# Performance work log

Measured on AMD Instinct MI355X. Metric: run time of the kernel, lower is better.

## Reference

```python
import jax, jax.numpy as jnp
import numpy as np

N, E, CLIP, HID, H, P, MD, B = 4096, 16384, 512, 1024, 4, 4, 512, 32
OUT2 = P * MD  # 2048


def prelu(x, a):
    return jnp.where(x >= 0, x, a * x)


def add_self_loops(src, dst, edge_attr, n):
    # PyG fill_value='mean': self-loop edge_attr = mean of incoming edge attrs
    sums = jax.ops.segment_sum(edge_attr, dst, num_segments=n)
    cnt = jax.ops.segment_sum(jnp.ones((dst.shape[0], 1), edge_attr.dtype), dst, num_segments=n)
    loop_attr = sums / jnp.maximum(cnt, 1.0)
    idx = jnp.arange(n)
    return (jnp.concatenate([src, idx]), jnp.concatenate([dst, idx]),
            jnp.concatenate([edge_attr, loop_attr], axis=0))


def gat_conv(x, src, dst, edge_attr, W, asrc, adst, We, ae, bias, heads, c):
    # PyG GATConv, concat=False (mean over heads), edge_dim used only in attention
    n = x.shape[0]
    src, dst, edge_attr = add_self_loops(src, dst, edge_attr, n)
    h = (x @ W).reshape(n, heads, c)                      # [N,H,C]
    e = (edge_attr @ We).reshape(-1, heads, c)            # [E',H,C]
    a_s = jnp.einsum('nhc,hc->nh', h, asrc)
    a_d = jnp.einsum('nhc,hc->nh', h, adst)
    a_e = jnp.einsum('ehc,hc->eh', e, ae)
    alpha = jax.nn.leaky_relu(a_s[src] + a_d[dst] + a_e, 0.2)  # [E',H]
    amax = jax.ops.segment_max(alpha, dst, num_segments=n)
    ex = jnp.exp(alpha - amax[dst])
    denom = jax.ops.segment_sum(ex, dst, num_segments=n)
    w = ex / jnp.maximum(denom[dst], 1e-16)
    msg = h[src] * w[:, :, None]                          # [E',H,C]
    out = jax.ops.segment_sum(msg, dst, num_segments=n)   # [N,H,C]
    return out.mean(axis=1) + bias


def attentional_pool(x, batch, gW1, gb1, gp1, gW2, gb2, gp2, gW3, gb3, n_graphs):
    gate = prelu(x @ gW1 + gb1, gp1)
    gate = prelu(gate @ gW2 + gb2, gp2)
    gate = gate @ gW3 + gb3                               # [N,1]
    gmax = jax.ops.segment_max(gate, batch, num_segments=n_graphs)
    ex = jnp.exp(gate - gmax[batch])
    denom = jax.ops.segment_sum(ex, batch, num_segments=n_graphs)
    s = ex / jnp.maximum(denom[batch], 1e-16)             # [N,1]
    return jax.ops.segment_sum(s * x, batch, num_segments=n_graphs)  # [B,F]


def setup_inputs() -> dict:
    key = jax.random.key(0)
    ks = jax.random.split(key, 24)
    sc = 0.05
    inp = {
        'x': jax.random.normal(ks[0], (N, CLIP), jnp.float32),
        'edge_index': jax.random.randint(ks[1], (2, E), 0, N),
        'edge_attr': jax.random.normal(ks[2], (E, CLIP), jnp.float32),
        'batch': jnp.sort(jax.random.randint(ks[3], (N,), 0, B)),
        # GATConv 1
        'W1': jax.random.normal(ks[4], (CLIP, H * HID), jnp.float32) * sc,
        'asrc1': jax.random.normal(ks[5], (H, HID), jnp.float32) * sc,
        'adst1': jax.random.normal(ks[6], (H, HID), jnp.float32) * sc,
        'We1': jax.random.normal(ks[7], (CLIP, H * HID), jnp.float32) * sc,
        'ae1': jax.random.normal(ks[8], (H, HID), jnp.float32) * sc,
        'b1': jnp.zeros((HID,), jnp.float32),
        'p1': jnp.float32(0.25),
        # GATConv 2
        'W2': jax.random.normal(ks[9], (HID, H * OUT2), jnp.float32) * sc,
        'asrc2': jax.random.normal(ks[10], (H, OUT2), jnp.float32) * sc,
        'adst2': jax.random.normal(ks[11], (H, OUT2), jnp.float32) * sc,
        'We2': jax.random.normal(ks[12], (CLIP, H * OUT2), jnp.float32) * sc,
        'ae2': jax.random.normal(ks[13], (H, OUT2), jnp.float32) * sc,
        'b2': jnp.zeros((OUT2,), jnp.float32),
        'p2': jnp.float32(0.25),
        # AttentionalAggregation gate_nn
        'gW1': jax.random.normal(ks[14], (OUT2, HID), jnp.float32) * sc,
        'gb1': jnp.zeros((HID,), jnp.float32),
        'gp1': jnp.float32(0.25),
        'gW2': jax.random.normal(ks[15], (HID, HID), jnp.float32) * sc,
        'gb2': jnp.zeros((HID,), jnp.float32),
        'gp2': jnp.float32(0.25),
        'gW3': jax.random.normal(ks[16], (HID, 1), jnp.float32) * sc,
        'gb3': jnp.zeros((1,), jnp.float32),
    }
    return inp


def reference(x, edge_index, edge_attr, batch,
              W1, asrc1, adst1, We1, ae1, b1, p1,
              W2, asrc2, adst2, We2, ae2, b2, p2,
              gW1, gb1, gp1, gW2, gb2, gp2, gW3, gb3):
    src, dst = edge_index[0], edge_index[1]
    h = gat_conv(x, src, dst, edge_attr, W1, asrc1, adst1, We1, ae1, b1, H, HID)
    h = prelu(h, p1)
    h = gat_conv(h, src, dst, edge_attr, W2, asrc2, adst2, We2, ae2, b2, H, OUT2)
    h = prelu(h, p2)
    pooled = attentional_pool(h, batch, gW1, gb1, gp1, gW2, gb2, gp2, gW3, gb3, B)
    return pooled.reshape(-1, P, MD)  # [B, prefix_length, mbart_dim]
```

## Files before the change

### kernel.cpp

```cpp
#include <hip/hip_runtime.h>
#include <hip/hip_bf16.h>
#include <math.h>

#define N_NODES 4096
#define N_EDGES 16384
#define CLIPD   512
#define HID     1024
#define NH      4
#define OUTD    2048
#define NB      32

typedef __bf16 bf16_t;
typedef bf16_t bf16x8 __attribute__((ext_vector_type(8)));
typedef float f32x4 __attribute__((ext_vector_type(4)));

static __device__ __forceinline__ float lrelu(float x) { return x >= 0.f ? x : 0.2f * x; }

static __device__ __forceinline__ unsigned short f2bf(float f) {
  union { float f; unsigned int u; } v; v.f = f;
  unsigned int u = v.u;
  unsigned int r = (u + 0x7FFFu + ((u >> 16) & 1u)) >> 16;
  return (unsigned short)r;
}
static __device__ __forceinline__ float bf2f(unsigned short u) {
  union { unsigned int i; float f; } v; v.i = ((unsigned int)u) << 16; return v.f;
}

#define GLDS(g, l) __builtin_amdgcn_global_load_lds( \
    (const __attribute__((address_space(1))) void*)(g), \
    (__attribute__((address_space(3))) void*)(l), 16, 0, 0)

__device__ __forceinline__ void stcvt_tile(float (*t)[33], const float* __restrict__ in,
                                           unsigned short* __restrict__ out,
                                           int K1, int N1, int NHH, int h, int bx, int by,
                                           float scale) {
  const int k0 = by * 32, n0 = bx * 32;
  const int tx = threadIdx.x, ty = threadIdx.y;
#pragma unroll
  for (int i = 0; i < 4; ++i)
    t[ty + 8 * i][tx] = in[(size_t)(k0 + ty + 8 * i) * (NHH * N1) + (size_t)h * N1 + n0 + tx];
  __syncthreads();
#pragma unroll
  for (int i = 0; i < 4; ++i)
    out[(size_t)(n0 + ty + 8 * i) * (NHH * K1) + (size_t)h * K1 + k0 + tx] =
        f2bf(scale * t[tx][ty + 8 * i]);
}

__global__ __launch_bounds__(256) void wprep_kernel(const float* __restrict__ W1, const float* __restrict__ W2,
                                                    const float* __restrict__ gW1, const float* __restrict__ gW2,
                                                    unsigned short* __restrict__ B1t, unsigned short* __restrict__ B2t,
                                                    unsigned short* __restrict__ gW1t, unsigned short* __restrict__ gW2t) {
  __shared__ float t[32][33];
  const int id = blockIdx.x;
  if (id < 2048) {
    int h = id >> 9, r = id & 511;
    stcvt_tile(t, W1, B1t, CLIPD, HID, NH, h, r & 31, r >> 5, 0.25f);
  } else if (id < 10240) {
    int r2 = id - 2048;
    int h = r2 >> 11, r = r2 & 2047;
    stcvt_tile(t, W2, B2t, HID, OUTD, NH, h, r & 63, r >> 6, 0.25f);
  } else if (id < 12288) {
    int r = id - 10240;
    stcvt_tile(t, gW1, gW1t, OUTD, HID, 1, 0, r & 31, r >> 5, 1.0f);
  } else {
    int r = id - 12288;
    stcvt_tile(t, gW2, gW2t, HID, HID, 1, 0, r & 31, r >> 5, 1.0f);
  }
}

__device__ __forceinline__ void vfold(float (*r1)[NH], float (*r2)[NH],
                                      const float* __restrict__ W,
                                      const float* __restrict__ a1v, const float* __restrict__ a2v,
                                      float* __restrict__ o1, float* __restrict__ o2, int C, int k) {
  const int tid = threadIdx.x;
  const float* row = W + (size_t)k * (NH * C);
  float x1[NH] = {0.f, 0.f, 0.f, 0.f}, x2[NH] = {0.f, 0.f, 0.f, 0.f};
  for (int c = tid; c < C; c += 256) {
    for (int h = 0; h < NH; ++h) {
      float w = row[h * C + c];
      x1[h] += w * a1v[h * C + c];
      x2[h] += w * a2v[h * C + c];
    }
  }
  for (int h = 0; h < NH; ++h)
    for (int o = 32; o > 0; o >>= 1) {
      x1[h] += __shfl_down(x1[h], o);
      x2[h] += __shfl_down(x2[h], o);
    }
  const int wid = tid >> 6, lane = tid & 63;
  if (lane == 0)
    for (int h = 0; h < NH; ++h) { r1[wid][h] = x1[h]; r2[wid][h] = x2[h]; }
  __syncthreads();
  if (tid < NH)
    o1[k * NH + tid] = r1[0][tid] + r1[1][tid] + r1[2][tid] + r1[3][tid];
  else if (o2 != nullptr && tid < 2 * NH) {
    int h = tid - NH;
    o2[k * NH + h] = r2[0][h] + r2[1][h] + r2[2][h] + r2[3][h];
  }
}

__global__ __launch_bounds__(256) void vprep_kernel(const float* __restrict__ We1, const float* __restrict__ ae1w,
                                                    const float* __restrict__ We2, const float* __restrict__ ae2w,
                                                    const float* __restrict__ W1, const float* __restrict__ asrc1,
                                                    const float* __restrict__ adst1,
                                                    const float* __restrict__ W2, const float* __restrict__ asrc2,
                                                    const float* __restrict__ adst2,
                                                    float* __restrict__ v1, float* __restrict__ v2,
                                                    float* __restrict__ us1, float* __restrict__ ud1,
                                                    float* __restrict__ us2, float* __restrict__ ud2) {
  __shared__ float r1[4][NH], r2[4][NH];
  const int id = blockIdx.x;
  if (id < 512)       vfold(r1, r2, We1, ae1w, ae1w, v1, nullptr, HID, id);
  else if (id < 1024) vfold(r1, r2, We2, ae2w, ae2w, v2, nullptr, OUTD, id - 512);
  else if (id < 1536) vfold(r1, r2, W1, asrc1, adst1, us1, ud1, HID, id - 1024);
  else                vfold(r1, r2, W2, asrc2, adst2, us2, ud2, OUTD, id - 1536);
}

__global__ __launch_bounds__(1024) void csr_kernel(const int* __restrict__ ei,
                                                   int* __restrict__ offs,
                                                   int* __restrict__ csr_src, int* __restrict__ csr_eid) {
  __shared__ int sdeg[N_NODES];
  __shared__ int soffs[N_NODES];
  __shared__ int sscan[1024];
  const int t = threadIdx.x;
  for (int i = t; i < N_NODES; i += 1024) sdeg[i] = 0;
  __syncthreads();
  for (int e = t; e < N_EDGES; e += 1024) atomicAdd(&sdeg[ei[N_EDGES + e]], 1);
  __syncthreads();
  const int d0 = sdeg[4 * t], d1 = sdeg[4 * t + 1], d2 = sdeg[4 * t + 2], d3 = sdeg[4 * t + 3];
  sscan[t] = d0 + d1 + d2 + d3;
  __syncthreads();
  for (int off = 1; off < 1024; off <<= 1) {
    int v = (t >= off) ? sscan[t - off] : 0;
    __syncthreads();
    sscan[t] += v;
    __syncthreads();
  }
  const int base = (t > 0) ? sscan[t - 1] : 0;
  soffs[4 * t] = base;
  soffs[4 * t + 1] = base + d0;
  soffs[4 * t + 2] = base + d0 + d1;
  soffs[4 * t + 3] = base + d0 + d1 + d2;
#pragma unroll
  for (int j = 0; j < 4; ++j) offs[4 * t + j] = soffs[4 * t + j];
  if (t == 1023) offs[N_NODES] = sscan[1023];
  sdeg[4 * t] = 0; sdeg[4 * t + 1] = 0; sdeg[4 * t + 2] = 0; sdeg[4 * t + 3] = 0;
  __syncthreads();
  for (int e = t; e < N_EDGES; e += 1024) {
    int dst = ei[N_EDGES + e];
    int pos = soffs[dst] + atomicAdd(&sdeg[dst], 1);
    csr_src[pos] = ei[e];
    csr_eid[pos] = e;
  }
}

__global__ __launch_bounds__(256) void ae_kernel(const float* __restrict__ ea, const int* __restrict__ ei,
                                                 const float* __restrict__ v1, const float* __restrict__ v2,
                                                 float* __restrict__ ae1, float* __restrict__ ae2,
                                                 float* __restrict__ aesum1, float* __restrict__ aesum2) {
  __shared__ float4 v1s[CLIPD];
  __shared__ float4 v2s[CLIPD];
  const int tid = threadIdx.x;
  v1s[tid] = ((const float4*)v1)[tid];
  v1s[tid + 256] = ((const float4*)v1)[tid + 256];
  v2s[tid] = ((const float4*)v2)[tid];
  v2s[tid + 256] = ((const float4*)v2)[tid + 256];
  __syncthreads();
  const int wid = tid >> 6, lane = tid & 63;
  for (int i = 0; i < 16; ++i) {
    const int e = blockIdx.x * 64 + wid * 16 + i;
    const float* row = ea + (size_t)e * CLIPD;
    float a1[NH] = {0.f, 0.f, 0.f, 0.f}, a2[NH] = {0.f, 0.f, 0.f, 0.f};
    for (int k = lane; k < CLIPD; k += 64) {
      float x = row[k];
      float4 w1 = v1s[k];
      float4 w2 = v2s[k];
      a1[0] += x * w1.x; a1[1] += x * w1.y; a1[2] += x * w1.z; a1[3] += x * w1.w;
      a2[0] += x * w2.x; a2[1] += x * w2.y; a2[2] += x * w2.z; a2[3] += x * w2.w;
    }
    for (int h = 0; h < NH; ++h)
      for (int o = 32; o > 0; o >>= 1) {
        a1[h] += __shfl_down(a1[h], o);
        a2[h] += __shfl_down(a2[h], o);
      }
    if (lane == 0) {
      int dst = ei[N_EDGES + e];
      for (int h = 0; h < NH; ++h) {
        ae1[e * NH + h] = a1[h];
        ae2[e * NH + h] = a2[h];
        atomicAdd(&aesum1[dst * NH + h], a1[h]);
        atomicAdd(&aesum2[dst * NH + h], a2[h]);
      }
    }
  }
}

__global__ __launch_bounds__(256) void xprep_kernel(const float* __restrict__ x,
                                                    const float* __restrict__ us, const float* __restrict__ ud,
                                                    unsigned short* __restrict__ xb,
                                                    float* __restrict__ as_, float* __restrict__ ad_) {
  __shared__ float4 su[CLIPD], sd[CLIPD];
  const int tid = threadIdx.x;
  for (int k = tid; k < CLIPD; k += 256) {
    su[k] = ((const float4*)us)[k];
    sd[k] = ((const float4*)ud)[k];
  }
  __syncthreads();
  const int wid = tid >> 6, lane = tid & 63;
  const int n = blockIdx.x * 4 + wid;
  const float* row = x + (size_t)n * CLIPD;
  unsigned short* orow = xb + (size_t)n * CLIPD;
  float s[NH] = {0.f, 0.f, 0.f, 0.f}, d[NH] = {0.f, 0.f, 0.f, 0.f};
  for (int q = lane; q < CLIPD / 4; q += 64) {
    float4 xv = ((const float4*)row)[q];
    ushort4 ob;
    ob.x = f2bf(xv.x); ob.y = f2bf(xv.y); ob.z = f2bf(xv.z); ob.w = f2bf(xv.w);
    ((ushort4*)orow)[q] = ob;
    const float* xp = &xv.x;
#pragma unroll
    for (int j = 0; j < 4; ++j) {
      float xs = xp[j];
      float4 u = su[q * 4 + j], v = sd[q * 4 + j];
      s[0] += xs * u.x; s[1] += xs * u.y; s[2] += xs * u.z; s[3] += xs * u.w;
      d[0] += xs * v.x; d[1] += xs * v.y; d[2] += xs * v.z; d[3] += xs * v.w;
    }
  }
#pragma unroll
  for (int h = 0; h < NH; ++h)
    for (int o = 32; o > 0; o >>= 1) {
      s[h] += __shfl_down(s[h], o);
      d[h] += __shfl_down(d[h], o);
    }
  if (lane == 0)
    for (int h = 0; h < NH; ++h) {
      as_[n * NH + h] = s[h];
      ad_[n * NH + h] = d[h];
    }
}

__global__ __launch_bounds__(256) void rowdot_o(const unsigned short* __restrict__ rows,
                                                const float* __restrict__ us, const float* __restrict__ ud,
                                                float* __restrict__ as_, float* __restrict__ ad_) {
  __shared__ float4 su[HID], sd[HID];
  const int tid = threadIdx.x;
  for (int k = tid; k < HID; k += 256) {
    su[k] = ((const float4*)us)[k];
    sd[k] = ((const float4*)ud)[k];
  }
  __syncthreads();
  const int wid = tid >> 6, lane = tid & 63;
  const int n = blockIdx.x * 4 + wid;
  const unsigned short* row = rows + (size_t)n * HID;
  float s[NH] = {0.f, 0.f, 0.f, 0.f}, d[NH] = {0.f, 0.f, 0.f, 0.f};
  for (int k2 = lane; k2 < HID / 2; k2 += 64) {
    ushort2 uv = ((const ushort2*)row)[k2];
    float f0 = bf2f(uv.x), f1 = bf2f(uv.y);
    float4 u0 = su[2 * k2], u1 = su[2 * k2 + 1];
    float4 v0 = sd[2 * k2], v1 = sd[2 * k2 + 1];
    s[0] += f0 * u0.x + f1 * u1.x; s[1] += f0 * u0.y + f1 * u1.y;
    s[2] += f0 * u0.z + f1 * u1.z; s[3] += f0 * u0.w + f1 * u1.w;
    d[0] += f0 * v0.x + f1 * v1.x; d[1] += f0 * v0.y + f1 * v1.y;
    d[2] += f0 * v0.z + f1 * v1.z; d[3] += f0 * v0.w + f1 * v1.w;
  }
#pragma unroll
  for (int h = 0; h < NH; ++h)
    for (int o = 32; o > 0; o >>= 1) {
      s[h] += __shfl_down(s[h], o);
      d[h] += __shfl_down(d[h], o);
    }
  if (lane == 0)
    for (int h = 0; h < NH; ++h) {
      as_[n * NH + h] = s[h];
      ad_[n * NH + h] = d[h];
    }
}

template<int C>
__global__ __launch_bounds__(256) void aggn_kernel(const unsigned short* __restrict__ src,
                                                   const float* __restrict__ as_, const float* __restrict__ ad_,
                                                   const float* __restrict__ aee, const float* __restrict__ aesum,
                                                   const int* __restrict__ offs, const int* __restrict__ csr_src,
                                                   const int* __restrict__ csr_eid,
                                                   unsigned short* __restrict__ out) {
  constexpr int CPT = C / 256;
  const int n = blockIdx.x;
  const int tid = threadIdx.x;
  const int off = offs[n];
  const int deg = offs[n + 1] - off;
  __shared__ float minv[NH], dinv[NH], wself[NH];
  __shared__ float wch[32][NH];
  __shared__ int sch[32];
  if (tid < 64) {
    const int h = tid >> 4, slot = tid & 15;
    const float adn = ad_[n * NH + h];
    const float aself = lrelu(as_[n * NH + h] + adn + aesum[n * NH + h] / fmaxf((float)deg, 1.f));
    float m = (slot == 0) ? aself : -3.0e38f;
    for (int i = slot; i < deg; i += 16) {
      float a = lrelu(as_[csr_src[off + i] * NH + h] + adn + aee[csr_eid[off + i] * NH + h]);
      m = fmaxf(m, a);
    }
    for (int o = 1; o < 16; o <<= 1) m = fmaxf(m, __shfl_xor(m, o));
    float den = (slot == 0) ? __expf(aself - m) : 0.f;
    for (int i = slot; i < deg; i += 16) {
      float a = lrelu(as_[csr_src[off + i] * NH + h] + adn + aee[csr_eid[off + i] * NH + h]);
      den += __expf(a - m);
    }
    for (int o = 1; o < 16; o <<= 1) den += __shfl_xor(den, o);
    if (slot == 0) {
      minv[h] = m;
      dinv[h] = 1.0f / den;
      wself[h] = __expf(aself - m) / den;
    }
  }
  __syncthreads();
  float acc[NH][CPT];
#pragma unroll
  for (int h = 0; h < NH; ++h)
#pragma unroll
    for (int c = 0; c < CPT; ++c) acc[h][c] = 0.f;
  for (int base = 0; base < deg; base += 32) {
    const int cnt = min(32, deg - base);
    if (tid < cnt * NH) {
      const int i = tid >> 2, h = tid & 3;
      const int sidx = csr_src[off + base + i];
      float a = lrelu(as_[sidx * NH + h] + ad_[n * NH + h] + aee[csr_eid[off + base + i] * NH + h]);
      wch[i][h] = __expf(a - minv[h]) * dinv[h];
      if (h == 0) sch[i] = sidx;
    }
    __syncthreads();
    for (int i = 0; i < cnt; ++i) {
      const unsigned short* hp = src + (size_t)sch[i] * C + tid * CPT;
      float f[CPT];
      if constexpr (CPT == 2) {
        ushort2 u = *(const ushort2*)hp;
        f[0] = bf2f(u.x); f[1] = bf2f(u.y);
      } else {
        ushort4 u = *(const ushort4*)hp;
        f[0] = bf2f(u.x); f[1] = bf2f(u.y); f[2] = bf2f(u.z); f[3] = bf2f(u.w);
      }
#pragma unroll
      for (int h = 0; h < NH; ++h) {
        const float wv = wch[i][h];
#pragma unroll
        for (int c = 0; c < CPT; ++c) acc[h][c] += wv * f[c];
      }
    }
    __syncthreads();
  }
  {
    const unsigned short* hp = src + (size_t)n * C + tid * CPT;
    float f[CPT];
    if constexpr (CPT == 2) {
      ushort2 u = *(const ushort2*)hp;
      f[0] = bf2f(u.x); f[1] = bf2f(u.y);
    } else {
      ushort4 u = *(const ushort4*)hp;
      f[0] = bf2f(u.x); f[1] = bf2f(u.y); f[2] = bf2f(u.z); f[3] = bf2f(u.w);
    }
#pragma unroll
    for (int h = 0; h < NH; ++h) {
      const float wv = wself[h];
#pragma unroll
      for (int c = 0; c < CPT; ++c) acc[h][c] += wv * f[c];
    }
  }
#pragma unroll
  for (int h = 0; h < NH; ++h) {
    if constexpr (CPT == 2) {
      ushort2 o;
      o.x = f2bf(acc[h][0]); o.y = f2bf(acc[h][1]);
      *(ushort2*)&out[((size_t)n * NH + h) * C + tid * 2] = o;
    } else {
      ushort4 o;
      o.x = f2bf(acc[h][0]); o.y = f2bf(acc[h][1]); o.z = f2bf(acc[h][2]); o.w = f2bf(acc[h][3]);
      *(ushort4*)&out[((size_t)n * NH + h) * C + tid * 4] = o;
    }
  }
}

template<int EPI, int WF, int BN>
__global__ __launch_bounds__(256) void mfma_gemm(const unsigned short* __restrict__ A,
                                                 const unsigned short* __restrict__ Bt,
                                                 unsigned short* __restrict__ C,
                                                 float* __restrict__ Cf,
                                                 int M, int N, int K,
                                                 const float* __restrict__ bias,
                                                 const float* __restrict__ pa) {
  constexpr int NFR = BN / 32;
  __shared__ unsigned short As[128 * 32];
  __shared__ unsigned short Bs[BN * 32];
  const int nwg = gridDim.x * gridDim.y;
  int id = blockIdx.y * gridDim.x + blockIdx.x;
  id = (id & 7) * (nwg >> 3) + (id >> 3);
  const int bx = id % gridDim.x, by = id / gridDim.x;
  const int tid = threadIdx.x;
  const int lane = tid & 63;
  const int w = tid >> 6;
  const int wr = w >> 1, wc = w & 1;
  const int brow = by * 128, bcol = bx * BN;
  const int r0 = tid >> 2;
  const int koff = (tid & 3) * 8;
  const int fr = lane & 15;
  const int fk = (lane >> 4) * 8;
  f32x4 acc[4][NFR] = {};
  for (int kt = 0; kt < K; kt += 32) {
    GLDS(A + (size_t)(brow + r0) * K + kt + koff, &As[tid * 8]);
    GLDS(A + (size_t)(brow + 64 + r0) * K + kt + koff, &As[2048 + tid * 8]);
    GLDS(Bt + (size_t)(bcol + r0) * K + kt + koff, &Bs[tid * 8]);
    if constexpr (BN == 128)
      GLDS(Bt + (size_t)(bcol + 64 + r0) * K + kt + koff, &Bs[2048 + tid * 8]);
    asm volatile("s_waitcnt vmcnt(0)" ::: "memory");
    __syncthreads();
    bf16x8 af[4], bfr[NFR];
#pragma unroll
    for (int mi = 0; mi < 4; ++mi)
      af[mi] = *(const bf16x8*)&As[(wr * 64 + mi * 16 + fr) * 32 + fk];
#pragma unroll
    for (int ni = 0; ni < NFR; ++ni)
      bfr[ni] = *(const bf16x8*)&Bs[(wc * (BN / 2) + ni * 16 + fr) * 32 + fk];
#pragma unroll
    for (int mi = 0; mi < 4; ++mi)
#pragma unroll
      for (int ni = 0; ni < NFR; ++ni)
        acc[mi][ni] = __builtin_amdgcn_mfma_f32_16x16x32_bf16(af[mi], bfr[ni], acc[mi][ni], 0, 0, 0);
    __syncthreads();
  }
  const float ap = EPI ? *pa : 0.f;
#pragma unroll
  for (int mi = 0; mi < 4; ++mi) {
    const int rb = brow + wr * 64 + mi * 16 + (lane >> 4) * 4;
#pragma unroll
    for (int ni = 0; ni < NFR; ++ni) {
      const int col = bcol + wc * (BN / 2) + ni * 16 + fr;
      float bv = 0.f;
      if (EPI) bv = bias[col];
#pragma unroll
      for (int r = 0; r < 4; ++r) {
        float v = acc[mi][ni][r];
        if (EPI) { v += bv; v = v >= 0.f ? v : ap * v; }
        C[(size_t)(rb + r) * N + col] = f2bf(v);
        if (WF) Cf[(size_t)(rb + r) * N + col] = v;
      }
    }
  }
}

__global__ __launch_bounds__(256) void gate3_kernel(const unsigned short* __restrict__ gh2,
                                                    const float* __restrict__ gW3,
                                                    const float* __restrict__ gb3, float* __restrict__ gate) {
  const int n = blockIdx.x, tid = threadIdx.x;
  const unsigned short* row = gh2 + (size_t)n * HID;
  ushort4 u = *(const ushort4*)&row[tid * 4];
  float4 wv = *(const float4*)&gW3[tid * 4];
  float acc = bf2f(u.x) * wv.x + bf2f(u.y) * wv.y + bf2f(u.z) * wv.z + bf2f(u.w) * wv.w;
  for (int o = 32; o > 0; o >>= 1) acc += __shfl_down(acc, o);
  __shared__ float red[4];
  const int wid = tid >> 6, lane = tid & 63;
  if (lane == 0) red[wid] = acc;
  __syncthreads();
  if (tid == 0) gate[n] = red[0] + red[1] + red[2] + red[3] + gb3[0];
}

__global__ __launch_bounds__(256) void pool2_kernel(const float* __restrict__ out2,
                                                    const float* __restrict__ gate,
                                                    const int* __restrict__ batch,
                                                    float* __restrict__ dout) {
  const int b = blockIdx.y;
  const int tid = threadIdx.x;
  const int col = blockIdx.x * 256 + tid;
  int lo = 0, hi = N_NODES;
  while (lo < hi) { int mid = (lo + hi) >> 1; if (batch[mid] < b) lo = mid + 1; else hi = mid; }
  const int s = lo;
  hi = N_NODES;
  while (lo < hi) { int mid = (lo + hi) >> 1; if (batch[mid] < b + 1) lo = mid + 1; else hi = mid; }
  const int e = lo;
  __shared__ float red[4];
  const int wid = tid >> 6, lane = tid & 63;
  float m = -3.0e38f;
  for (int n = s + tid; n < e; n += 256) m = fmaxf(m, gate[n]);
  for (int o = 32; o > 0; o >>= 1) m = fmaxf(m, __shfl_down(m, o));
  if (lane == 0) red[wid] = m;
  __syncthreads();
  m = fmaxf(fmaxf(red[0], red[1]), fmaxf(red[2], red[3]));
  __syncthreads();
  float sum = 0.f;
  for (int n = s + tid; n < e; n += 256) sum += __expf(gate[n] - m);
  for (int o = 32; o > 0; o >>= 1) sum += __shfl_down(sum, o);
  if (lane == 0) red[wid] = sum;
  __syncthreads();
  sum = red[0] + red[1] + red[2] + red[3];
  const float gi = 1.0f / fmaxf(sum, 1e-16f);
  float acc = 0.f;
  for (int n = s; n < e; ++n)
    acc += __expf(gate[n] - m) * gi * out2[(size_t)n * OUTD + col];
  dout[(size_t)b * OUTD + col] = acc;
}

#define MB(x) ((size_t)(x) * 1048576)
#define WS_XB     MB(0)
#define WS_B1T    MB(4)
#define WS_B2T    MB(8)
#define WS_GW1T   MB(24)
#define WS_GW2T   MB(28)
#define WS_AGGX   MB(30)
#define WS_OUT1B  MB(46)
#define WS_AGGO   MB(54)
#define WS_OUT2F  MB(86)
#define WS_OUT2B  MB(118)
#define WS_GH1B   MB(134)
#define WS_GH2B   MB(142)
#define WS_SM     MB(150)
#define WS_AES1   (WS_SM + 0)
#define WS_AES2   (WS_AES1 + 65536)
#define WS_OFFS   (WS_AES2 + 65536)
#define WS_CSRS   (WS_OFFS + 16640)
#define WS_CSRE   (WS_CSRS + 65536)
#define WS_AS1    (WS_CSRE + 65536)
#define WS_AD1    (WS_AS1 + 65536)
#define WS_AEE1   (WS_AD1 + 65536)
#define WS_AS2    (WS_AEE1 + 262144)
#define WS_AD2    (WS_AS2 + 65536)
#define WS_AEE2   (WS_AD2 + 65536)
#define WS_V1     (WS_AEE2 + 262144)
#define WS_V2     (WS_V1 + 8192)
#define WS_US1    (WS_V2 + 8192)
#define WS_UD1    (WS_US1 + 8192)
#define WS_US2    (WS_UD1 + 8192)
#define WS_UD2    (WS_US2 + 16384)
#define WS_GATE   (WS_UD2 + 16384)

extern "C" void kernel_launch(void* const* d_in, const int* in_sizes, int n_in,
                              void* d_out, int out_size, void* d_ws, size_t ws_size,
                              hipStream_t stream) {
  const float* x     = (const float*)d_in[0];
  const int*   ei    = (const int*)d_in[1];
  const float* ea    = (const float*)d_in[2];
  const int*   batch = (const int*)d_in[3];
  const float* W1    = (const float*)d_in[4];
  const float* asrc1 = (const float*)d_in[5];
  const float* adst1 = (const float*)d_in[6];
  const float* We1   = (const float*)d_in[7];
  const float* ae1w  = (const float*)d_in[8];
  const float* b1    = (const float*)d_in[9];
  const float* p1    = (const float*)d_in[10];
  const float* W2    = (const float*)d_in[11];
  const float* asrc2 = (const float*)d_in[12];
  const float* adst2 = (const float*)d_in[13];
  const float* We2   = (const float*)d_in[14];
  const float* ae2w  = (const float*)d_in[15];
  const float* b2    = (const float*)d_in[16];
  const float* p2    = (const float*)d_in[17];
  const float* gW1   = (const float*)d_in[18];
  const float* gb1   = (const float*)d_in[19];
  const float* gp1   = (const float*)d_in[20];
  const float* gW2   = (const float*)d_in[21];
  const float* gb2   = (const float*)d_in[22];
  const float* gp2   = (const float*)d_in[23];
  const float* gW3   = (const float*)d_in[24];
  const float* gb3   = (const float*)d_in[25];

  char* ws = (char*)d_ws;
  unsigned short* xb    = (unsigned short*)(ws + WS_XB);
  unsigned short* B1t   = (unsigned short*)(ws + WS_B1T);
  unsigned short* B2t   = (unsigned short*)(ws + WS_B2T);
  unsigned short* gW1t  = (unsigned short*)(ws + WS_GW1T);
  unsigned short* gW2t  = (unsigned short*)(ws + WS_GW2T);
  unsigned short* aggXb = (unsigned short*)(ws + WS_AGGX);
  unsigned short* out1b = (unsigned short*)(ws + WS_OUT1B);
  unsigned short* aggOb = (unsigned short*)(ws + WS_AGGO);
  float*          out2f = (float*)(ws + WS_OUT2F);
  unsigned short* out2b = (unsigned short*)(ws + WS_OUT2B);
  unsigned short* gh1b  = (unsigned short*)(ws + WS_GH1B);
  unsigned short* gh2b  = (unsigned short*)(ws + WS_GH2B);
  float* aesum1  = (float*)(ws + WS_AES1);
  float* aesum2  = (float*)(ws + WS_AES2);
  int*   offs    = (int*)(ws + WS_OFFS);
  int*   csr_src = (int*)(ws + WS_CSRS);
  int*   csr_eid = (int*)(ws + WS_CSRE);
  float* as1     = (float*)(ws + WS_AS1);
  float* ad1     = (float*)(ws + WS_AD1);
  float* aee1    = (float*)(ws + WS_AEE1);
  float* as2     = (float*)(ws + WS_AS2);
  float* ad2     = (float*)(ws + WS_AD2);
  float* aee2    = (float*)(ws + WS_AEE2);
  float* v1      = (float*)(ws + WS_V1);
  float* v2      = (float*)(ws + WS_V2);
  float* us1     = (float*)(ws + WS_US1);
  float* ud1     = (float*)(ws + WS_UD1);
  float* us2     = (float*)(ws + WS_US2);
  float* ud2     = (float*)(ws + WS_UD2);
  float* gate    = (float*)(ws + WS_GATE);
  float* dout    = (float*)d_out;

  hipMemsetAsync(ws + WS_AES1, 0, 131072, stream);

  wprep_kernel<<<13312, dim3(32, 8), 0, stream>>>(W1, W2, gW1, gW2, B1t, B2t, gW1t, gW2t);
  vprep_kernel<<<2560, 256, 0, stream>>>(We1, ae1w, We2, ae2w, W1, asrc1, adst1, W2, asrc2, adst2,
                                         v1, v2, us1, ud1, us2, ud2);
  csr_kernel<<<1, 1024, 0, stream>>>(ei, offs, csr_src, csr_eid);
  ae_kernel<<<N_EDGES / 64, 256, 0, stream>>>(ea, ei, v1, v2, aee1, aee2, aesum1, aesum2);
  xprep_kernel<<<N_NODES / 4, 256, 0, stream>>>(x, us1, ud1, xb, as1, ad1);

  aggn_kernel<CLIPD><<<N_NODES, 256, 0, stream>>>(xb, as1, ad1, aee1, aesum1, offs, csr_src, csr_eid, aggXb);
  mfma_gemm<1, 0, 64><<<dim3(HID / 64, N_NODES / 128), 256, 0, stream>>>(
      aggXb, B1t, out1b, nullptr, N_NODES, HID, NH * CLIPD, b1, p1);

  rowdot_o<<<N_NODES / 4, 256, 0, stream>>>(out1b, us2, ud2, as2, ad2);
  aggn_kernel<HID><<<N_NODES, 256, 0, stream>>>(out1b, as2, ad2, aee2, aesum2, offs, csr_src, csr_eid, aggOb);
  mfma_gemm<1, 1, 128><<<dim3(OUTD / 128, N_NODES / 128), 256, 0, stream>>>(
      aggOb, B2t, out2b, out2f, N_NODES, OUTD, NH * HID, b2, p2);

  mfma_gemm<1, 0, 64><<<dim3(HID / 64, N_NODES / 128), 256, 0, stream>>>(
      out2b, gW1t, gh1b, nullptr, N_NODES, HID, OUTD, gb1, gp1);
  mfma_gemm<1, 0, 64><<<dim3(HID / 64, N_NODES / 128), 256, 0, stream>>>(
      gh1b, gW2t, gh2b, nullptr, N_NODES, HID, HID, gb2, gp2);
  gate3_kernel<<<N_NODES, 256, 0, stream>>>(gh2b, gW3, gb3, gate);

  pool2_kernel<<<dim3(OUTD / 256, NB), 256, 0, stream>>>(out2f, gate, batch, dout);
}
```

Before: 543.7 us.

## Merge prep kernels, wave-per-node aggregation, fuse gate projection into GEMM epilogue

Merges the weight-transpose and vector-fold prep kernels into one launch, and the edge-attention and x-prep kernels into another. Node aggregation now uses one wave per node with 16-byte bf16 loads instead of a 256-thread block with LDS staging and barriers. The final 1-wide gate projection is folded into the second gate GEMM's epilogue through shuffle reductions and atomicAdd, which removes the gh2 buffer and the gate3 kernel. The gb3 bias is dropped because the pooling softmax does not change under a constant shift. The second GAT GEMM tile width also changes from 128 to 64. These changes target launch count, extra memory traffic and per-node sync cost, at the price of float atomic contention on the gate values and possibly lower GEMM reuse.

```diff
diff --git a/kernel.cpp b/kernel.cpp
--- a/kernel.cpp
+++ b/kernel.cpp
@@ -13,6 +13,7 @@
 typedef __bf16 bf16_t;
 typedef bf16_t bf16x8 __attribute__((ext_vector_type(8)));
 typedef float f32x4 __attribute__((ext_vector_type(4)));
+typedef unsigned short u16x8 __attribute__((ext_vector_type(8)));
 
 static __device__ __forceinline__ float lrelu(float x) { return x >= 0.f ? x : 0.2f * x; }
 
@@ -35,7 +36,7 @@
                                            int K1, int N1, int NHH, int h, int bx, int by,
                                            float scale) {
   const int k0 = by * 32, n0 = bx * 32;
-  const int tx = threadIdx.x, ty = threadIdx.y;
+  const int tx = threadIdx.x & 31, ty = threadIdx.x >> 5;
 #pragma unroll
   for (int i = 0; i < 4; ++i)
     t[ty + 8 * i][tx] = in[(size_t)(k0 + ty + 8 * i) * (NHH * N1) + (size_t)h * N1 + n0 + tx];
@@ -44,28 +45,6 @@
   for (int i = 0; i < 4; ++i)
     out[(size_t)(n0 + ty + 8 * i) * (NHH * K1) + (size_t)h * K1 + k0 + tx] =
         f2bf(scale * t[tx][ty + 8 * i]);
-}
-
-__global__ __launch_bounds__(256) void wprep_kernel(const float* __restrict__ W1, const float* __restrict__ W2,
-                                                    const float* __restrict__ gW1, const float* __restrict__ gW2,
-                                                    unsigned short* __restrict__ B1t, unsigned short* __restrict__ B2t,
-                                                    unsigned short* __restrict__ gW1t, unsigned short* __restrict__ gW2t) {
-  __shared__ float t[32][33];
-  const int id = blockIdx.x;
-  if (id < 2048) {
-    int h = id >> 9, r = id & 511;
-    stcvt_tile(t, W1, B1t, CLIPD, HID, NH, h, r & 31, r >> 5, 0.25f);
-  } else if (id < 10240) {
-    int r2 = id - 2048;
-    int h = r2 >> 11, r = r2 & 2047;
-    stcvt_tile(t, W2, B2t, HID, OUTD, NH, h, r & 63, r >> 6, 0.25f);
-  } else if (id < 12288) {
-    int r = id - 10240;
-    stcvt_tile(t, gW1, gW1t, OUTD, HID, 1, 0, r & 31, r >> 5, 1.0f);
-  } else {
-    int r = id - 12288;
-    stcvt_tile(t, gW2, gW2t, HID, HID, 1, 0, r & 31, r >> 5, 1.0f);
-  }
 }
 
 __device__ __forceinline__ void vfold(float (*r1)[NH], float (*r2)[NH],
@@ -99,21 +78,41 @@
   }
 }
 
-__global__ __launch_bounds__(256) void vprep_kernel(const float* __restrict__ We1, const float* __restrict__ ae1w,
-                                                    const float* __restrict__ We2, const float* __restrict__ ae2w,
-                                                    const float* __restrict__ W1, const float* __restrict__ asrc1,
-                                                    const float* __restrict__ adst1,
-                                                    const float* __restrict__ W2, const float* __restrict__ asrc2,
-                                                    const float* __restrict__ adst2,
-                                                    float* __restrict__ v1, float* __restrict__ v2,
-                                                    float* __restrict__ us1, float* __restrict__ ud1,
-                                                    float* __restrict__ us2, float* __restrict__ ud2) {
+__global__ __launch_bounds__(256) void prep_kernel(
+    const float* __restrict__ W1, const float* __restrict__ W2,
+    const float* __restrict__ gW1, const float* __restrict__ gW2,
+    unsigned short* __restrict__ B1t, unsigned short* __restrict__ B2t,
+    unsigned short* __restrict__ gW1t, unsigned short* __restrict__ gW2t,
+    const float* __restrict__ We1, const float* __restrict__ ae1w,
+    const float* __restrict__ We2, const float* __restrict__ ae2w,
+    const float* __restrict__ asrc1, const float* __restrict__ adst1,
+    const float* __restrict__ asrc2, const float* __restrict__ adst2,
+    float* __restrict__ v1, float* __restrict__ v2,
+    float* __restrict__ us1, float* __restrict__ ud1,
+    float* __restrict__ us2, float* __restrict__ ud2) {
+  __shared__ float t[32][33];
   __shared__ float r1[4][NH], r2[4][NH];
   const int id = blockIdx.x;
-  if (id < 512)       vfold(r1, r2, We1, ae1w, ae1w, v1, nullptr, HID, id);
-  else if (id < 1024) vfold(r1, r2, We2, ae2w, ae2w, v2, nullptr, OUTD, id - 512);
-  else if (id < 1536) vfold(r1, r2, W1, asrc1, adst1, us1, ud1, HID, id - 1024);
-  else                vfold(r1, r2, W2, asrc2, adst2, us2, ud2, OUTD, id - 1536);
+  if (id < 2048) {
+    int h = id >> 9, r = id & 511;
+    stcvt_tile(t, W1, B1t, CLIPD, HID, NH, h, r & 31, r >> 5, 0.25f);
+  } else if (id < 10240) {
+    int r2_ = id - 2048;
+    int h = r2_ >> 11, r = r2_ & 2047;
+    stcvt_tile(t, W2, B2t, HID, OUTD, NH, h, r & 63, r >> 6, 0.25f);
+  } else if (id < 12288) {
+    int r = id - 10240;
+    stcvt_tile(t, gW1, gW1t, OUTD, HID, 1, 0, r & 31, r >> 5, 1.0f);
+  } else if (id < 13312) {
+    int r = id - 12288;
+    stcvt_tile(t, gW2, gW2t, HID, HID, 1, 0, r & 31, r >> 5, 1.0f);
+  } else {
+    int vid = id - 13312;
+    if (vid < 512)       vfold(r1, r2, We1, ae1w, ae1w, v1, nullptr, HID, vid);
+    else if (vid < 1024) vfold(r1, r2, We2, ae2w, ae2w, v2, nullptr, OUTD, vid - 512);
+    else if (vid < 1536) vfold(r1, r2, W1, asrc1, adst1, us1, ud1, HID, vid - 1024);
+    else                 vfold(r1, r2, W2, asrc2, adst2, us2, ud2, OUTD, vid - 1536);
+  }
 }
 
 __global__ __launch_bounds__(1024) void csr_kernel(const int* __restrict__ ei,
@@ -154,88 +153,85 @@
   }
 }
 
-__global__ __launch_bounds__(256) void ae_kernel(const float* __restrict__ ea, const int* __restrict__ ei,
-                                                 const float* __restrict__ v1, const float* __restrict__ v2,
-                                                 float* __restrict__ ae1, float* __restrict__ ae2,
-                                                 float* __restrict__ aesum1, float* __restrict__ aesum2) {
-  __shared__ float4 v1s[CLIPD];
-  __shared__ float4 v2s[CLIPD];
+__global__ __launch_bounds__(256) void aexprep_kernel(
+    const float* __restrict__ ea, const int* __restrict__ ei,
+    const float* __restrict__ v1, const float* __restrict__ v2,
+    float* __restrict__ ae1, float* __restrict__ ae2,
+    float* __restrict__ aesum1, float* __restrict__ aesum2,
+    const float* __restrict__ x, const float* __restrict__ us, const float* __restrict__ ud,
+    unsigned short* __restrict__ xb, float* __restrict__ as_, float* __restrict__ ad_) {
+  __shared__ float4 s0[CLIPD];
+  __shared__ float4 s1[CLIPD];
   const int tid = threadIdx.x;
-  v1s[tid] = ((const float4*)v1)[tid];
-  v1s[tid + 256] = ((const float4*)v1)[tid + 256];
-  v2s[tid] = ((const float4*)v2)[tid];
-  v2s[tid + 256] = ((const float4*)v2)[tid + 256];
-  __syncthreads();
   const int wid = tid >> 6, lane = tid & 63;
-  for (int i = 0; i < 16; ++i) {
-    const int e = blockIdx.x * 64 + wid * 16 + i;
-    const float* row = ea + (size_t)e * CLIPD;
-    float a1[NH] = {0.f, 0.f, 0.f, 0.f}, a2[NH] = {0.f, 0.f, 0.f, 0.f};
-    for (int k = lane; k < CLIPD; k += 64) {
-      float x = row[k];
-      float4 w1 = v1s[k];
-      float4 w2 = v2s[k];
-      a1[0] += x * w1.x; a1[1] += x * w1.y; a1[2] += x * w1.z; a1[3] += x * w1.w;
-      a2[0] += x * w2.x; a2[1] += x * w2.y; a2[2] += x * w2.z; a2[3] += x * w2.w;
-    }
+  if (blockIdx.x < 256) {
+    s0[tid] = ((const float4*)v1)[tid];
+    s0[tid + 256] = ((const float4*)v1)[tid + 256];
+    s1[tid] = ((const float4*)v2)[tid];
+    s1[tid + 256] = ((const float4*)v2)[tid + 256];
+    __syncthreads();
+    for (int i = 0; i < 16; ++i) {
+      const int e = blockIdx.x * 64 + wid * 16 + i;
+      const float* row = ea + (size_t)e * CLIPD;
+      float a1[NH] = {0.f, 0.f, 0.f, 0.f}, a2[NH] = {0.f, 0.f, 0.f, 0.f};
+      for (int k = lane; k < CLIPD; k += 64) {
+        float xv = row[k];
+        float4 w1 = s0[k];
+        float4 w2 = s1[k];
+        a1[0] += xv * w1.x; a1[1] += xv * w1.y; a1[2] += xv * w1.z; a1[3] += xv * w1.w;
+        a2[0] += xv * w2.x; a2[1] += xv * w2.y; a2[2] += xv * w2.z; a2[3] += xv * w2.w;
+      }
+      for (int h = 0; h < NH; ++h)
+        for (int o = 32; o > 0; o >>= 1) {
+          a1[h] += __shfl_down(a1[h], o);
+          a2[h] += __shfl_down(a2[h], o);
+        }
+      if (lane == 0) {
+        int dst = ei[N_EDGES + e];
+        for (int h = 0; h < NH; ++h) {
+          ae1[e * NH + h] = a1[h];
+          ae2[e * NH + h] = a2[h];
+          atomicAdd(&aesum1[dst * NH + h], a1[h]);
+          atomicAdd(&aesum2[dst * NH + h], a2[h]);
+        }
+      }
+    }
+  } else {
+    for (int k = tid; k < CLIPD; k += 256) {
+      s0[k] = ((const float4*)us)[k];
+      s1[k] = ((const float4*)ud)[k];
+    }
+    __syncthreads();
+    const int n = (blockIdx.x - 256) * 4 + wid;
+    const float* row = x + (size_t)n * CLIPD;
+    unsigned short* orow = xb + (size_t)n * CLIPD;
+    float s[NH] = {0.f, 0.f, 0.f, 0.f}, d[NH] = {0.f, 0.f, 0.f, 0.f};
+    for (int q = lane; q < CLIPD / 4; q += 64) {
+      float4 xv = ((const float4*)row)[q];
+      ushort4 ob;
+      ob.x = f2bf(xv.x); ob.y = f2bf(xv.y); ob.z = f2bf(xv.z); ob.w = f2bf(xv.w);
+      ((ushort4*)orow)[q] = ob;
+      const float* xp = &xv.x;
+#pragma unroll
+      for (int j = 0; j < 4; ++j) {
+        float xs = xp[j];
+        float4 u = s0[q * 4 + j], v = s1[q * 4 + j];
+        s[0] += xs * u.x; s[1] += xs * u.y; s[2] += xs * u.z; s[3] += xs * u.w;
+        d[0] += xs * v.x; d[1] += xs * v.y; d[2] += xs * v.z; d[3] += xs * v.w;
+      }
+    }
+#pragma unroll
     for (int h = 0; h < NH; ++h)
       for (int o = 32; o > 0; o >>= 1) {
-        a1[h] += __shfl_down(a1[h], o);
-        a2[h] += __shfl_down(a2[h], o);
-      }
-    if (lane == 0) {
-      int dst = ei[N_EDGES + e];
+        s[h] += __shfl_down(s[h], o);
+        d[h] += __shfl_down(d[h], o);
+      }
+    if (lane == 0)
       for (int h = 0; h < NH; ++h) {
-        ae1[e * NH + h] = a1[h];
-        ae2[e * NH + h] = a2[h];
-        atomicAdd(&aesum1[dst * NH + h], a1[h]);
-        atomicAdd(&aesum2[dst * NH + h], a2[h]);
-      }
-    }
-  }
-}
-
-__global__ __launch_bounds__(256) void xprep_kernel(const float* __restrict__ x,
-                                                    const float* __restrict__ us, const float* __restrict__ ud,
-                                                    unsigned short* __restrict__ xb,
-                                                    float* __restrict__ as_, float* __restrict__ ad_) {
-  __shared__ float4 su[CLIPD], sd[CLIPD];
-  const int tid = threadIdx.x;
-  for (int k = tid; k < CLIPD; k += 256) {
-    su[k] = ((const float4*)us)[k];
-    sd[k] = ((const float4*)ud)[k];
-  }
-  __syncthreads();
-  const int wid = tid >> 6, lane = tid & 63;
-  const int n = blockIdx.x * 4 + wid;
-  const float* row = x + (size_t)n * CLIPD;
-  unsigned short* orow = xb + (size_t)n * CLIPD;
-  float s[NH] = {0.f, 0.f, 0.f, 0.f}, d[NH] = {0.f, 0.f, 0.f, 0.f};
-  for (int q = lane; q < CLIPD / 4; q += 64) {
-    float4 xv = ((const float4*)row)[q];
-    ushort4 ob;
-    ob.x = f2bf(xv.x); ob.y = f2bf(xv.y); ob.z = f2bf(xv.z); ob.w = f2bf(xv.w);
-    ((ushort4*)orow)[q] = ob;
-    const float* xp = &xv.x;
-#pragma unroll
-    for (int j = 0; j < 4; ++j) {
-      float xs = xp[j];
-      float4 u = su[q * 4 + j], v = sd[q * 4 + j];
-      s[0] += xs * u.x; s[1] += xs * u.y; s[2] += xs * u.z; s[3] += xs * u.w;
-      d[0] += xs * v.x; d[1] += xs * v.y; d[2] += xs * v.z; d[3] += xs * v.w;
-    }
-  }
-#pragma unroll
-  for (int h = 0; h < NH; ++h)
-    for (int o = 32; o > 0; o >>= 1) {
-      s[h] += __shfl_down(s[h], o);
-      d[h] += __shfl_down(d[h], o);
-    }
-  if (lane == 0)
-    for (int h = 0; h < NH; ++h) {
-      as_[n * NH + h] = s[h];
-      ad_[n * NH + h] = d[h];
-    }
+        as_[n * NH + h] = s[h];
+        ad_[n * NH + h] = d[h];
+      }
+  }
 }
 
 __global__ __launch_bounds__(256) void rowdot_o(const unsigned short* __restrict__ rows,
@@ -276,116 +272,107 @@
 }
 
 template<int C>
-__global__ __launch_bounds__(256) void aggn_kernel(const unsigned short* __restrict__ src,
+__global__ __launch_bounds__(256) void aggw_kernel(const unsigned short* __restrict__ src,
                                                    const float* __restrict__ as_, const float* __restrict__ ad_,
                                                    const float* __restrict__ aee, const float* __restrict__ aesum,
                                                    const int* __restrict__ offs, const int* __restrict__ csr_src,
                                                    const int* __restrict__ csr_eid,
                                                    unsigned short* __restrict__ out) {
-  constexpr int CPT = C / 256;
-  const int n = blockIdx.x;
-  const int tid = threadIdx.x;
+  constexpr int CPT = C / 64;
+  const int lane = threadIdx.x & 63;
+  const int n = blockIdx.x * 4 + (threadIdx.x >> 6);
   const int off = offs[n];
   const int deg = offs[n + 1] - off;
-  __shared__ float minv[NH], dinv[NH], wself[NH];
-  __shared__ float wch[32][NH];
-  __shared__ int sch[32];
-  if (tid < 64) {
-    const int h = tid >> 4, slot = tid & 15;
-    const float adn = ad_[n * NH + h];
-    const float aself = lrelu(as_[n * NH + h] + adn + aesum[n * NH + h] / fmaxf((float)deg, 1.f));
-    float m = (slot == 0) ? aself : -3.0e38f;
-    for (int i = slot; i < deg; i += 16) {
-      float a = lrelu(as_[csr_src[off + i] * NH + h] + adn + aee[csr_eid[off + i] * NH + h]);
-      m = fmaxf(m, a);
-    }
-    for (int o = 1; o < 16; o <<= 1) m = fmaxf(m, __shfl_xor(m, o));
-    float den = (slot == 0) ? __expf(aself - m) : 0.f;
-    for (int i = slot; i < deg; i += 16) {
-      float a = lrelu(as_[csr_src[off + i] * NH + h] + adn + aee[csr_eid[off + i] * NH + h]);
-      den += __expf(a - m);
-    }
-    for (int o = 1; o < 16; o <<= 1) den += __shfl_xor(den, o);
-    if (slot == 0) {
-      minv[h] = m;
-      dinv[h] = 1.0f / den;
-      wself[h] = __expf(aself - m) / den;
-    }
-  }
-  __syncthreads();
+  const int h = lane >> 4, slot = lane & 15;
+  const float4 ad4 = *(const float4*)&ad_[n * NH];
+  const float4 as4 = *(const float4*)&as_[n * NH];
+  const float4 ae4 = *(const float4*)&aesum[n * NH];
+  const float adn = ((const float*)&ad4)[h];
+  const float aself = lrelu(((const float*)&as4)[h] + adn +
+                            ((const float*)&ae4)[h] / fmaxf((float)deg, 1.f));
+  float m = (slot == 0) ? aself : -3.0e38f;
+  for (int i = slot; i < deg; i += 16) {
+    float a = lrelu(as_[csr_src[off + i] * NH + h] + adn + aee[csr_eid[off + i] * NH + h]);
+    m = fmaxf(m, a);
+  }
+#pragma unroll
+  for (int o = 1; o < 16; o <<= 1) m = fmaxf(m, __shfl_xor(m, o));
+  float den = (slot == 0) ? __expf(aself - m) : 0.f;
+  for (int i = slot; i < deg; i += 16) {
+    float a = lrelu(as_[csr_src[off + i] * NH + h] + adn + aee[csr_eid[off + i] * NH + h]);
+    den += __expf(a - m);
+  }
+#pragma unroll
+  for (int o = 1; o < 16; o <<= 1) den += __shfl_xor(den, o);
+  const float wself_l = __expf(aself - m) / den;
+  float mh[NH], dh[NH], wsh[NH];
+#pragma unroll
+  for (int hh = 0; hh < NH; ++hh) {
+    mh[hh] = __shfl(m, hh * 16);
+    dh[hh] = 1.0f / __shfl(den, hh * 16);
+    wsh[hh] = __shfl(wself_l, hh * 16);
+  }
   float acc[NH][CPT];
 #pragma unroll
-  for (int h = 0; h < NH; ++h)
-#pragma unroll
-    for (int c = 0; c < CPT; ++c) acc[h][c] = 0.f;
-  for (int base = 0; base < deg; base += 32) {
-    const int cnt = min(32, deg - base);
-    if (tid < cnt * NH) {
-      const int i = tid >> 2, h = tid & 3;
-      const int sidx = csr_src[off + base + i];
-      float a = lrelu(as_[sidx * NH + h] + ad_[n * NH + h] + aee[csr_eid[off + base + i] * NH + h]);
-      wch[i][h] = __expf(a - minv[h]) * dinv[h];
-      if (h == 0) sch[i] = sidx;
-    }
-    __syncthreads();
-    for (int i = 0; i < cnt; ++i) {
-      const unsigned short* hp = src + (size_t)sch[i] * C + tid * CPT;
-      float f[CPT];
-      if constexpr (CPT == 2) {
-        ushort2 u = *(const ushort2*)hp;
-        f[0] = bf2f(u.x); f[1] = bf2f(u.y);
-      } else {
-        ushort4 u = *(const ushort4*)hp;
-        f[0] = bf2f(u.x); f[1] = bf2f(u.y); f[2] = bf2f(u.z); f[3] = bf2f(u.w);
-      }
-#pragma unroll
-      for (int h = 0; h < NH; ++h) {
-        const float wv = wch[i][h];
-#pragma unroll
-        for (int c = 0; c < CPT; ++c) acc[h][c] += wv * f[c];
-      }
-    }
-    __syncthreads();
+  for (int hh = 0; hh < NH; ++hh)
+#pragma unroll
+    for (int c = 0; c < CPT; ++c) acc[hh][c] = 0.f;
+  for (int i = 0; i < deg; ++i) {
+    const int sidx = csr_src[off + i];
+    const float4 asv = *(const float4*)&as_[sidx * NH];
+    const float4 aev = *(const float4*)&aee[csr_eid[off + i] * NH];
+    float w[NH];
+#pragma unroll
+    for (int hh = 0; hh < NH; ++hh)
+      w[hh] = __expf(lrelu(((const float*)&asv)[hh] + ((const float*)&ad4)[hh] +
+                           ((const float*)&aev)[hh]) - mh[hh]) * dh[hh];
+    const unsigned short* hp = src + (size_t)sidx * C + lane * CPT;
+#pragma unroll
+    for (int v8 = 0; v8 < CPT / 8; ++v8) {
+      u16x8 u = *(const u16x8*)(hp + v8 * 8);
+#pragma unroll
+      for (int c = 0; c < 8; ++c) {
+        float f = bf2f(u[c]);
+#pragma unroll
+        for (int hh = 0; hh < NH; ++hh) acc[hh][v8 * 8 + c] += w[hh] * f;
+      }
+    }
   }
   {
-    const unsigned short* hp = src + (size_t)n * C + tid * CPT;
-    float f[CPT];
-    if constexpr (CPT == 2) {
-      ushort2 u = *(const ushort2*)hp;
-      f[0] = bf2f(u.x); f[1] = bf2f(u.y);
-    } else {
-      ushort4 u = *(const ushort4*)hp;
-      f[0] = bf2f(u.x); f[1] = bf2f(u.y); f[2] = bf2f(u.z); f[3] = bf2f(u.w);
-    }
-#pragma unroll
-    for (int h = 0; h < NH; ++h) {
-      const float wv = wself[h];
-#pragma unroll
-      for (int c = 0; c < CPT; ++c) acc[h][c] += wv * f[c];
-    }
-  }
-#pragma unroll
-  for (int h = 0; h < NH; ++h) {
-    if constexpr (CPT == 2) {
-      ushort2 o;
-      o.x = f2bf(acc[h][0]); o.y = f2bf(acc[h][1]);
-      *(ushort2*)&out[((size_t)n * NH + h) * C + tid * 2] = o;
-    } else {
-      ushort4 o;
-      o.x = f2bf(acc[h][0]); o.y = f2bf(acc[h][1]); o.z = f2bf(acc[h][2]); o.w = f2bf(acc[h][3]);
-      *(ushort4*)&out[((size_t)n * NH + h) * C + tid * 4] = o;
-    }
-  }
-}
-
-template<int EPI, int WF, int BN>
+    const unsigned short* hp = src + (size_t)n * C + lane * CPT;
+#pragma unroll
+    for (int v8 = 0; v8 < CPT / 8; ++v8) {
+      u16x8 u = *(const u16x8*)(hp + v8 * 8);
+#pragma unroll
+      for (int c = 0; c < 8; ++c) {
+        float f = bf2f(u[c]);
+#pragma unroll
+        for (int hh = 0; hh < NH; ++hh) acc[hh][v8 * 8 + c] += wsh[hh] * f;
+      }
+    }
+  }
+#pragma unroll
+  for (int hh = 0; hh < NH; ++hh) {
+#pragma unroll
+    for (int v8 = 0; v8 < CPT / 8; ++v8) {
+      u16x8 o;
+#pragma unroll
+      for (int c = 0; c < 8; ++c) o[c] = f2bf(acc[hh][v8 * 8 + c]);
+      *(u16x8*)&out[((size_t)n * NH + hh) * C + lane * CPT + v8 * 8] = o;
+    }
+  }
+}
+
+template<int EPI, int WF, int BN, int GATE>
 __global__ __launch_bounds__(256) void mfma_gemm(const unsigned short* __restrict__ A,
                                                  const unsigned short* __restrict__ Bt,
                                                  unsigned short* __restrict__ C,
                                                  float* __restrict__ Cf,
                                                  int M, int N, int K,
                                                  const float* __restrict__ bias,
-                                                 const float* __restrict__ pa) {
+                                                 const float* __restrict__ pa,
+                                                 const float* __restrict__ g3,
+                                                 float* __restrict__ gate) {
   constexpr int NFR = BN / 32;
   __shared__ unsigned short As[128 * 32];
   __shared__ unsigned short Bs[BN * 32];
@@ -426,39 +413,45 @@
     __syncthreads();
   }
   const float ap = EPI ? *pa : 0.f;
+  float g3v[NFR];
+  if constexpr (GATE) {
+#pragma unroll
+    for (int ni = 0; ni < NFR; ++ni) g3v[ni] = g3[bcol + wc * (BN / 2) + ni * 16 + fr];
+  }
 #pragma unroll
   for (int mi = 0; mi < 4; ++mi) {
     const int rb = brow + wr * 64 + mi * 16 + (lane >> 4) * 4;
-#pragma unroll
-    for (int ni = 0; ni < NFR; ++ni) {
-      const int col = bcol + wc * (BN / 2) + ni * 16 + fr;
-      float bv = 0.f;
-      if (EPI) bv = bias[col];
+    if constexpr (GATE) {
 #pragma unroll
       for (int r = 0; r < 4; ++r) {
-        float v = acc[mi][ni][r];
-        if (EPI) { v += bv; v = v >= 0.f ? v : ap * v; }
-        C[(size_t)(rb + r) * N + col] = f2bf(v);
-        if (WF) Cf[(size_t)(rb + r) * N + col] = v;
-      }
-    }
-  }
-}
-
-__global__ __launch_bounds__(256) void gate3_kernel(const unsigned short* __restrict__ gh2,
-                                                    const float* __restrict__ gW3,
-                                                    const float* __restrict__ gb3, float* __restrict__ gate) {
-  const int n = blockIdx.x, tid = threadIdx.x;
-  const unsigned short* row = gh2 + (size_t)n * HID;
-  ushort4 u = *(const ushort4*)&row[tid * 4];
-  float4 wv = *(const float4*)&gW3[tid * 4];
-  float acc = bf2f(u.x) * wv.x + bf2f(u.y) * wv.y + bf2f(u.z) * wv.z + bf2f(u.w) * wv.w;
-  for (int o = 32; o > 0; o >>= 1) acc += __shfl_down(acc, o);
-  __shared__ float red[4];
-  const int wid = tid >> 6, lane = tid & 63;
-  if (lane == 0) red[wid] = acc;
-  __syncthreads();
-  if (tid == 0) gate[n] = red[0] + red[1] + red[2] + red[3] + gb3[0];
+        float p = 0.f;
+#pragma unroll
+        for (int ni = 0; ni < NFR; ++ni) {
+          const int col = bcol + wc * (BN / 2) + ni * 16 + fr;
+          float v = acc[mi][ni][r] + bias[col];
+          v = v >= 0.f ? v : ap * v;
+          p += v * g3v[ni];
+        }
+#pragma unroll
+        for (int o = 1; o < 16; o <<= 1) p += __shfl_xor(p, o);
+        if (fr == 0) atomicAdd(&gate[rb + r], p);
+      }
+    } else {
+#pragma unroll
+      for (int ni = 0; ni < NFR; ++ni) {
+        const int col = bcol + wc * (BN / 2) + ni * 16 + fr;
+        float bv = 0.f;
+        if (EPI) bv = bias[col];
+#pragma unroll
+        for (int r = 0; r < 4; ++r) {
+          float v = acc[mi][ni][r];
+          if (EPI) { v += bv; v = v >= 0.f ? v : ap * v; }
+          C[(size_t)(rb + r) * N + col] = f2bf(v);
+          if (WF) Cf[(size_t)(rb + r) * N + col] = v;
+        }
+      }
+    }
+  }
 }
 
 __global__ __launch_bounds__(256) void pool2_kernel(const float* __restrict__ out2,
@@ -508,11 +501,12 @@
 #define WS_OUT2F  MB(86)
 #define WS_OUT2B  MB(118)
 #define WS_GH1B   MB(134)
-#define WS_GH2B   MB(142)
-#define WS_SM     MB(150)
+#define WS_SM     MB(142)
 #define WS_AES1   (WS_SM + 0)
 #define WS_AES2   (WS_AES1 + 65536)
-#define WS_OFFS   (WS_AES2 + 65536)
+#define WS_GATE   (WS_AES2 + 65536)
+#define WS_ZBYTES 147456
+#define WS_OFFS   (WS_GATE + 16384)
 #define WS_CSRS   (WS_OFFS + 16640)
 #define WS_CSRE   (WS_CSRS + 65536)
 #define WS_AS1    (WS_CSRE + 65536)
@@ -527,7 +521,6 @@
 #define WS_UD1    (WS_US1 + 8192)
 #define WS_US2    (WS_UD1 + 8192)
 #define WS_UD2    (WS_US2 + 16384)
-#define WS_GATE   (WS_UD2 + 16384)
 
 extern "C" void kernel_launch(void* const* d_in, const int* in_sizes, int n_in,
                               void* d_out, int out_size, void* d_ws, size_t ws_size,
@@ -557,7 +550,6 @@
   const float* gb2   = (const float*)d_in[22];
   const float* gp2   = (const float*)d_in[23];
   const float* gW3   = (const float*)d_in[24];
-  const float* gb3   = (const float*)d_in[25];
 
   char* ws = (char*)d_ws;
   unsigned short* xb    = (unsigned short*)(ws + WS_XB);
@@ -571,9 +563,9 @@
   float*          out2f = (float*)(ws + WS_OUT2F);
   unsigned short* out2b = (unsigned short*)(ws + WS_OUT2B);
   unsigned short* gh1b  = (unsigned short*)(ws + WS_GH1B);
-  unsigned short* gh2b  = (unsigned short*)(ws + WS_GH2B);
   float* aesum1  = (float*)(ws + WS_AES1);
   float* aesum2  = (float*)(ws + WS_AES2);
+  float* gate    = (float*)(ws + WS_GATE);
   int*   offs    = (int*)(ws + WS_OFFS);
   int*   csr_src = (int*)(ws + WS_CSRS);
   int*   csr_eid = (int*)(ws + WS_CSRE);
@@ -589,32 +581,32 @@
   float* ud1     = (float*)(ws + WS_UD1);
   float* us2     = (float*)(ws + WS_US2);
   float* ud2     = (float*)(ws + WS_UD2);
-  float* gate    = (float*)(ws + WS_GATE);
   float* dout    = (float*)d_out;
 
-  hipMemsetAsync(ws + WS_AES1, 0, 131072, stream);
-
-  wprep_kernel<<<13312, dim3(32, 8), 0, stream>>>(W1, W2, gW1, gW2, B1t, B2t, gW1t, gW2t);
-  vprep_kernel<<<2560, 256, 0, stream>>>(We1, ae1w, We2, ae2w, W1, asrc1, adst1, W2, asrc2, adst2,
+  hipMemsetAsync(ws + WS_AES1, 0, WS_ZBYTES, stream);
+
+  csr_kernel<<<1, 1024, 0, stream>>>(ei, offs, csr_src, csr_eid);
+  prep_kernel<<<15872, 256, 0, stream>>>(W1, W2, gW1, gW2, B1t, B2t, gW1t, gW2t,
+                                         We1, ae1w, We2, ae2w, asrc1, adst1, asrc2, adst2,
                                          v1, v2, us1, ud1, us2, ud2);
-  csr_kernel<<<1, 1024, 0, stream>>>(ei, offs, csr_src, csr_eid);
-  ae_kernel<<<N_EDGES / 64, 256, 0, stream>>>(ea, ei, v1, v2, aee1, aee2, aesum1, aesum2);
-  xprep_kernel<<<N_NODES / 4, 256, 0, stream>>>(x, us1, ud1, xb, as1, ad1);
-
-  aggn_kernel<CLIPD><<<N_NODES, 256, 0, stream>>>(xb, as1, ad1, aee1, aesum1, offs, csr_src, csr_eid, aggXb);
-  mfma_gemm<1, 0, 64><<<dim3(HID / 64, N_NODES / 128), 256, 0, stream>>>(
-      aggXb, B1t, out1b, nullptr, N_NODES, HID, NH * CLIPD, b1, p1);
+  aexprep_kernel<<<1280, 256, 0, stream>>>(ea, ei, v1, v2, aee1, aee2, aesum1, aesum2,
+                                           x, us1, ud1, xb, as1, ad1);
+
+  aggw_kernel<CLIPD><<<N_NODES / 4, 256, 0, stream>>>(xb, as1, ad1, aee1, aesum1,
+                                                      offs, csr_src, csr_eid, aggXb);
+  mfma_gemm<1, 0, 64, 0><<<dim3(HID / 64, N_NODES / 128), 256, 0, stream>>>(
+      aggXb, B1t, out1b, nullptr, N_NODES, HID, NH * CLIPD, b1, p1, nullptr, nullptr);
 
   rowdot_o<<<N_NODES / 4, 256, 0, stream>>>(out1b, us2, ud2, as2, ad2);
-  aggn_kernel<HID><<<N_NODES, 256, 0, stream>>>(out1b, as2, ad2, aee2, aesum2, offs, csr_src, csr_eid, aggOb);
-  mfma_gemm<1, 1, 128><<<dim3(OUTD / 128, N_NODES / 128), 256, 0, stream>>>(
-      aggOb, B2t, out2b, out2f, N_NODES, OUTD, NH * HID, b2, p2);
-
-  mfma_gemm<1, 0, 64><<<dim3(HID / 64, N_NODES / 128), 256, 0, stream>>>(
-      out2b, gW1t, gh1b, nullptr, N_NODES, HID, OUTD, gb1, gp1);
-  mfma_gemm<1, 0, 64><<<dim3(HID / 64, N_NODES / 128), 256, 0, stream>>>(
-      gh1b, gW2t, gh2b, nullptr, N_NODES, HID, HID, gb2, gp2);
-  gate3_kernel<<<N_NODES, 256, 0, stream>>>(gh2b, gW3, gb3, gate);
+  aggw_kernel<HID><<<N_NODES / 4, 256, 0, stream>>>(out1b, as2, ad2, aee2, aesum2,
+                                                    offs, csr_src, csr_eid, aggOb);
+  mfma_gemm<1, 1, 64, 0><<<dim3(OUTD / 64, N_NODES / 128), 256, 0, stream>>>(
+      aggOb, B2t, out2b, out2f, N_NODES, OUTD, NH * HID, b2, p2, nullptr, nullptr);
+
+  mfma_gemm<1, 0, 64, 0><<<dim3(HID / 64, N_NODES / 128), 256, 0, stream>>>(
+      out2b, gW1t, gh1b, nullptr, N_NODES, HID, OUTD, gb1, gp1, nullptr, nullptr);
+  mfma_gemm<1, 0, 64, 1><<<dim3(HID / 64, N_NODES / 128), 256, 0, stream>>>(
+      gh1b, gW2t, nullptr, nullptr, N_NODES, HID, HID, gb2, gp2, gW3, gate);
 
   pool2_kernel<<<dim3(OUTD / 256, NB), 256, 0, stream>>>(out2f, gate, batch, dout);
 }
```

Measured after the change: 587.0 us. 8.0% more time.
